# Optimization experiments

Measured on AMD Instinct MI355X. Metric: run time of the kernel, lower is better.

The kernel has to match this reference:

```python
import jax, jax.numpy as jnp
import numpy as np

D_MODEL = 1024
N_HEADS = 16
HEAD_DIM = D_MODEL // N_HEADS


def setup_inputs() -> dict:
    key = jax.random.key(0)
    ks = jax.random.split(key, 9)
    scale = 1.0 / np.sqrt(D_MODEL)
    x = jax.random.normal(ks[0], (2, 2048, D_MODEL), dtype=jnp.float32)
    Wq = jax.random.normal(ks[1], (D_MODEL, D_MODEL), dtype=jnp.float32) * scale
    bq = jax.random.normal(ks[2], (D_MODEL,), dtype=jnp.float32) * scale
    Wk = jax.random.normal(ks[3], (D_MODEL, D_MODEL), dtype=jnp.float32) * scale
    bk = jax.random.normal(ks[4], (D_MODEL,), dtype=jnp.float32) * scale
    Wv = jax.random.normal(ks[5], (D_MODEL, D_MODEL), dtype=jnp.float32) * scale
    bv = jax.random.normal(ks[6], (D_MODEL,), dtype=jnp.float32) * scale
    Wo = jax.random.normal(ks[7], (D_MODEL, D_MODEL), dtype=jnp.float32) * scale
    bo = jax.random.normal(ks[8], (D_MODEL,), dtype=jnp.float32) * scale
    return {"x": x, "Wq": Wq, "bq": bq, "Wk": Wk, "bk": bk,
            "Wv": Wv, "bv": bv, "Wo": Wo, "bo": bo}


def reference(x, Wq, bq, Wk, bk, Wv, bv, Wo, bo):
    B, S, _ = x.shape
    # projections: [B, S, D] -> [B, S, H, Dh]
    q = (x @ Wq + bq).reshape(B, S, N_HEADS, HEAD_DIM)
    k = (x @ Wk + bk).reshape(B, S, N_HEADS, HEAD_DIM)
    v = (x @ Wv + bv).reshape(B, S, N_HEADS, HEAD_DIM)
    inv_sqrt_d = jnp.float32(1.0 / np.sqrt(HEAD_DIM))
    # scores: [B, H, S, S]  (NOTE: source applies no causal mask despite name)
    scores = jnp.einsum('bqhd,bkhd->bhqk', q, k) * inv_sqrt_d
    attn = jax.nn.softmax(scores, axis=-1)
    out = jnp.einsum('bhqk,bkhd->bqhd', attn, v).reshape(B, S, D_MODEL)
    return out @ Wo + bo
```

## Files before the change

kernel.cpp:

```cpp
#include <hip/hip_runtime.h>

typedef __bf16 bf16x8 __attribute__((ext_vector_type(8)));
typedef float f32x4 __attribute__((ext_vector_type(4)));

#define D_MODEL 1024
#define SEQ 2048
#define NH 16
#define DH 64
#define MROWS 4096

__device__ __forceinline__ void load_lds16(const void* g, void* l) {
  __builtin_amdgcn_global_load_lds((__attribute__((address_space(1))) void*)g,
                                   (__attribute__((address_space(3))) void*)l, 16, 0, 0);
}

__device__ __forceinline__ f32x4 mfma16(bf16x8 a, bf16x8 b, f32x4 c) {
  return __builtin_amdgcn_mfma_f32_16x16x32_bf16(a, b, c, 0, 0, 0);
}

__device__ __forceinline__ unsigned pack2(float a, float b) {
  union { __bf16 h; unsigned short u; } pa, pb;
  pa.h = (__bf16)a; pb.h = (__bf16)b;
  return (unsigned)pa.u | ((unsigned)pb.u << 16);
}

__global__ __launch_bounds__(256) void cast_x_kernel(const float* __restrict__ X,
                                                     __bf16* __restrict__ Xb) {
  const size_t i = (size_t)blockIdx.x * 256 + threadIdx.x;
  const float4 a = reinterpret_cast<const float4*>(X)[i * 2];
  const float4 b = reinterpret_cast<const float4*>(X)[i * 2 + 1];
  bf16x8 o;
  o[0] = (__bf16)a.x; o[1] = (__bf16)a.y; o[2] = (__bf16)a.z; o[3] = (__bf16)a.w;
  o[4] = (__bf16)b.x; o[5] = (__bf16)b.y; o[6] = (__bf16)b.z; o[7] = (__bf16)b.w;
  *reinterpret_cast<bf16x8*>(Xb + i * 8) = o;
}

__global__ __launch_bounds__(256) void transpose_w(const float* __restrict__ W0, const float* __restrict__ W1,
                                                   const float* __restrict__ W2, const float* __restrict__ W3,
                                                   __bf16* __restrict__ WT) {
  __shared__ __bf16 tile[64][68];
  const int z = blockIdx.z;
  const float* W = z == 0 ? W0 : (z == 1 ? W1 : (z == 2 ? W2 : W3));
  const int r0 = blockIdx.x * 64;
  const int c0 = blockIdx.y * 64;
  const int tx = threadIdx.x & 63, ty = threadIdx.x >> 6;
#pragma unroll
  for (int i = 0; i < 16; ++i) {
    const int r = i * 4 + ty;
    tile[r][tx] = (__bf16)W[(size_t)(r0 + r) * D_MODEL + c0 + tx];
  }
  __syncthreads();
  __bf16* out = WT + (size_t)z * D_MODEL * D_MODEL;
#pragma unroll
  for (int i = 0; i < 16; ++i) {
    const int n = i * 4 + ty;
    out[(size_t)(c0 + n) * D_MODEL + r0 + tx] = tile[tx][n];
  }
}

template <int MODE>
__global__ __launch_bounds__(256) void gemm_bf16(
    const __bf16* __restrict__ A, const __bf16* __restrict__ BT,
    const float* __restrict__ bias0, const float* __restrict__ bias1, const float* __restrict__ bias2,
    __bf16* __restrict__ qout, __bf16* __restrict__ kout, __bf16* __restrict__ vout,
    float* __restrict__ fout) {
  __shared__ __bf16 As[128 * 32];
  __shared__ __bf16 Bs[128 * 32];
  const int t = threadIdx.x;
  const int l = t & 63;
  const int w = t >> 6;
  const int m0 = blockIdx.x * 128;
  const int n0 = blockIdx.y * 128;
  const int wr = w >> 1, wc = w & 1;
  const int l15 = l & 15, lhi = l >> 4;

  f32x4 acc[4][4] = {};

  const int srow = t >> 2;
  const int sslot = t & 3;

  for (int kt = 0; kt < D_MODEL / 32; ++kt) {
    const int kofs = kt * 32 + sslot * 8;
#pragma unroll
    for (int p = 0; p < 2; ++p) {
      load_lds16(A + (size_t)(m0 + p * 64 + srow) * D_MODEL + kofs, &As[(p * 64 + w * 16) * 32]);
      load_lds16(BT + (size_t)(n0 + p * 64 + srow) * D_MODEL + kofs, &Bs[(p * 64 + w * 16) * 32]);
    }
    __syncthreads();
    bf16x8 af[4], bfr[4];
#pragma unroll
    for (int i = 0; i < 4; ++i) {
      af[i] = *reinterpret_cast<const bf16x8*>(&As[(wr * 64 + i * 16 + l15) * 32 + lhi * 8]);
      bfr[i] = *reinterpret_cast<const bf16x8*>(&Bs[(wc * 64 + i * 16 + l15) * 32 + lhi * 8]);
    }
#pragma unroll
    for (int i = 0; i < 4; ++i)
#pragma unroll
      for (int j = 0; j < 4; ++j)
        acc[i][j] = mfma16(af[i], bfr[j], acc[i][j]);
    __syncthreads();
  }

  if (MODE == 0) {
#pragma unroll
    for (int j = 0; j < 4; ++j) {
      const int n = n0 + wc * 64 + j * 16 + l15;
      const int tsel = n >> 10;
      const int c = n & 1023;
      const float* bias = tsel == 0 ? bias0 : (tsel == 1 ? bias1 : bias2);
      const float bv = bias[c];
      const int h = c >> 6, dh = c & 63;
      if (tsel == 2) {
#pragma unroll
        for (int i = 0; i < 4; ++i) {
          const int mbase = m0 + wr * 64 + i * 16 + lhi * 4;
#pragma unroll
          for (int r = 0; r < 4; ++r) {
            const int mm = mbase + r;
            const int b = mm >> 11, s = mm & 2047;
            vout[((size_t)((b * NH + h) * DH + dh)) * SEQ + s] = (__bf16)(acc[i][j][r] + bv);
          }
        }
      } else {
        __bf16* dst = tsel == 0 ? qout : kout;
        const float scale = tsel == 0 ? 0.125f : 1.0f;
#pragma unroll
        for (int i = 0; i < 4; ++i) {
          const int mbase = m0 + wr * 64 + i * 16 + lhi * 4;
#pragma unroll
          for (int r = 0; r < 4; ++r) {
            const int mm = mbase + r;
            const int b = mm >> 11, s = mm & 2047;
            dst[((size_t)((b * NH + h) * SEQ + s)) * DH + dh] = (__bf16)((acc[i][j][r] + bv) * scale);
          }
        }
      }
    }
  } else {
#pragma unroll
    for (int j = 0; j < 4; ++j) {
      const int n = n0 + wc * 64 + j * 16 + l15;
      const float bv = bias0[n];
#pragma unroll
      for (int i = 0; i < 4; ++i) {
        const int mbase = m0 + wr * 64 + i * 16 + lhi * 4;
#pragma unroll
        for (int r = 0; r < 4; ++r)
          fout[(size_t)(mbase + r) * D_MODEL + n] = acc[i][j][r] + bv;
      }
    }
  }
}

__global__ __launch_bounds__(256) void flash_attn3(const __bf16* __restrict__ Q,
                                                   const __bf16* __restrict__ K,
                                                   const __bf16* __restrict__ VT,
                                                   __bf16* __restrict__ AO) {
  __shared__ __bf16 Kt[64 * 64];
  __shared__ __bf16 Vt[64 * 64];
  __shared__ __bf16 Pt[4][1024];
  const int t = threadIdx.x;
  const int l = t & 63, w = t >> 6;
  const int l15 = l & 15, lhi = l >> 4;

  const int fid = blockIdx.x;
  const int u = (fid & 7) * 128 + (fid >> 3);
  const int bh = u >> 5;
  const int qblk = u & 31;
  const int q0 = qblk * 64 + w * 16;

  const __bf16* Qb = Q + (size_t)bh * SEQ * DH;
  const __bf16* Kb = K + (size_t)bh * SEQ * DH;
  const __bf16* Vb = VT + (size_t)bh * DH * SEQ;

  bf16x8 qf[2];
#pragma unroll
  for (int kd = 0; kd < 2; ++kd)
    qf[kd] = *reinterpret_cast<const bf16x8*>(Qb + (size_t)(q0 + l15) * DH + kd * 32 + lhi * 8);

  f32x4 acc_o[4] = {};
  float mrun = -1e30f, lrun = 0.f;

  const int srow = l >> 3, sslot = l & 7;

  for (int kt = 0; kt < SEQ / 64; ++kt) {
    const int key0 = kt * 64;
#pragma unroll
    for (int pp = 0; pp < 2; ++pp) {
      const int p = w * 2 + pp;
      const int row = p * 8 + srow;
      const int sl = sslot ^ (row & 7);
      load_lds16(Kb + (size_t)(key0 + row) * DH + sl * 8, &Kt[p * 512]);
      load_lds16(Vb + (size_t)row * SEQ + key0 + sl * 8, &Vt[p * 512]);
    }
    __syncthreads();

    f32x4 s[4] = {};
#pragma unroll
    for (int kd = 0; kd < 2; ++kd)
#pragma unroll
      for (int kf = 0; kf < 4; ++kf) {
        const int key = kf * 16 + l15;
        const bf16x8 kfr = *reinterpret_cast<const bf16x8*>(
            &Kt[key * 64 + (((kd * 4 + lhi) ^ (key & 7)) << 3)]);
        s[kf] = mfma16(kfr, qf[kd], s[kf]);
      }

    float mt = s[0][0];
#pragma unroll
    for (int kf = 0; kf < 4; ++kf)
#pragma unroll
      for (int r = 0; r < 4; ++r) mt = fmaxf(mt, s[kf][r]);
    mt = fmaxf(mt, __shfl_xor(mt, 16));
    mt = fmaxf(mt, __shfl_xor(mt, 32));
    const float mnew = fmaxf(mrun, mt);
    const float alpha = __expf(mrun - mnew);
    float sum = 0.f;
#pragma unroll
    for (int kf = 0; kf < 4; ++kf)
#pragma unroll
      for (int r = 0; r < 4; ++r) {
        const float p = __expf(s[kf][r] - mnew);
        s[kf][r] = p;
        sum += p;
      }
    sum += __shfl_xor(sum, 16);
    sum += __shfl_xor(sum, 32);
    lrun = lrun * alpha + sum;
    mrun = mnew;
#pragma unroll
    for (int d0 = 0; d0 < 4; ++d0)
#pragma unroll
      for (int r = 0; r < 4; ++r) acc_o[d0][r] *= alpha;

#pragma unroll
    for (int kf = 0; kf < 4; ++kf) {
      uint2 wv;
      wv.x = pack2(s[kf][0], s[kf][1]);
      wv.y = pack2(s[kf][2], s[kf][3]);
      const int blk = (kf >> 1) * 4 + (kf & 1) * 2 + (lhi >> 1);
      const int dw = ((blk * 16 + l15) << 2) + ((lhi & 1) << 1);
      *reinterpret_cast<uint2*>(&Pt[w][dw * 2]) = wv;
    }

#pragma unroll
    for (int kc = 0; kc < 2; ++kc) {
      const bf16x8 pfr = *reinterpret_cast<const bf16x8*>(&Pt[w][((kc * 4 + lhi) * 16 + l15) * 8]);
#pragma unroll
      for (int d0 = 0; d0 < 4; ++d0) {
        const int dh = d0 * 16 + l15;
        const bf16x8 vfr = *reinterpret_cast<const bf16x8*>(
            &Vt[dh * 64 + (((kc * 4 + lhi) ^ (dh & 7)) << 3)]);
        acc_o[d0] = mfma16(vfr, pfr, acc_o[d0]);
      }
    }
    __syncthreads();
  }

  const int b = bh >> 4, h = bh & 15;
  const int s_ = q0 + l15;
  const float inv = 1.0f / lrun;
  __bf16* aorow = AO + ((size_t)(b * SEQ + s_)) * D_MODEL + h * DH;
#pragma unroll
  for (int d0 = 0; d0 < 4; ++d0) {
    const int dh0 = d0 * 16 + lhi * 4;
    uint2 pk;
    pk.x = pack2(acc_o[d0][0] * inv, acc_o[d0][1] * inv);
    pk.y = pack2(acc_o[d0][2] * inv, acc_o[d0][3] * inv);
    *reinterpret_cast<uint2*>(aorow + dh0) = pk;
  }
}

extern "C" void kernel_launch(void* const* d_in, const int* in_sizes, int n_in,
                              void* d_out, int out_size, void* d_ws, size_t ws_size,
                              hipStream_t stream) {
  (void)in_sizes; (void)n_in; (void)out_size; (void)ws_size;
  const float* x  = (const float*)d_in[0];
  const float* Wq = (const float*)d_in[1];
  const float* bq = (const float*)d_in[2];
  const float* Wk = (const float*)d_in[3];
  const float* bk = (const float*)d_in[4];
  const float* Wv = (const float*)d_in[5];
  const float* bv = (const float*)d_in[6];
  const float* Wo = (const float*)d_in[7];
  const float* bo = (const float*)d_in[8];
  float* out = (float*)d_out;
  char* ws = (char*)d_ws;
  __bf16* xb = (__bf16*)(ws);
  __bf16* WT = (__bf16*)(ws + (8u << 20));
  __bf16* qb = (__bf16*)(ws + (16u << 20));
  __bf16* kb = (__bf16*)(ws + (24u << 20));
  __bf16* vb = (__bf16*)(ws + (32u << 20));
  __bf16* ao = (__bf16*)(ws + (40u << 20));

  cast_x_kernel<<<dim3(2048), dim3(256), 0, stream>>>(x, xb);
  transpose_w<<<dim3(16, 16, 4), dim3(256), 0, stream>>>(Wq, Wk, Wv, Wo, WT);
  gemm_bf16<0><<<dim3(32, 24), dim3(256), 0, stream>>>(xb, WT, bq, bk, bv, qb, kb, vb, nullptr);
  flash_attn3<<<dim3(1024), dim3(256), 0, stream>>>(qb, kb, vb, ao);
  gemm_bf16<1><<<dim3(32, 8), dim3(256), 0, stream>>>(ao, WT + (size_t)3072 * 1024, bo,
                                                      nullptr, nullptr, nullptr, nullptr, nullptr, out);
}
```

Baseline: 229.6 us.

## Double-buffer attention K/V tiles, use exp2 with lazy rescaling, stage V-transpose store via LDS

Result: faster. 222.3 us (-3.2%).

```diff
diff --git a/kernel.cpp b/kernel.cpp
--- a/kernel.cpp
+++ b/kernel.cpp
@@ -8,6 +8,7 @@
 #define NH 16
 #define DH 64
 #define MROWS 4096
+#define LOG2E 1.44269504088896340736f
 
 __device__ __forceinline__ void load_lds16(const void* g, void* l) {
   __builtin_amdgcn_global_load_lds((__attribute__((address_space(1))) void*)g,
@@ -64,8 +65,9 @@
     const float* __restrict__ bias0, const float* __restrict__ bias1, const float* __restrict__ bias2,
     __bf16* __restrict__ qout, __bf16* __restrict__ kout, __bf16* __restrict__ vout,
     float* __restrict__ fout) {
-  __shared__ __bf16 As[128 * 32];
-  __shared__ __bf16 Bs[128 * 32];
+  __shared__ __bf16 sm[2][128 * 32];
+  __bf16* As = sm[0];
+  __bf16* Bs = sm[1];
   const int t = threadIdx.x;
   const int l = t & 63;
   const int w = t >> 6;
@@ -102,28 +104,52 @@
   }
 
   if (MODE == 0) {
-#pragma unroll
-    for (int j = 0; j < 4; ++j) {
-      const int n = n0 + wc * 64 + j * 16 + l15;
-      const int tsel = n >> 10;
-      const int c = n & 1023;
-      const float* bias = tsel == 0 ? bias0 : (tsel == 1 ? bias1 : bias2);
-      const float bv = bias[c];
-      const int h = c >> 6, dh = c & 63;
-      if (tsel == 2) {
-#pragma unroll
-        for (int i = 0; i < 4; ++i) {
-          const int mbase = m0 + wr * 64 + i * 16 + lhi * 4;
-#pragma unroll
-          for (int r = 0; r < 4; ++r) {
-            const int mm = mbase + r;
-            const int b = mm >> 11, s = mm & 2047;
-            vout[((size_t)((b * NH + h) * DH + dh)) * SEQ + s] = (__bf16)(acc[i][j][r] + bv);
+    if (n0 >= 2048) {
+      __bf16* Ts = sm[0];
+      char* Tsb = reinterpret_cast<char*>(Ts);
+      const int b = m0 >> 11, s0m = m0 & 2047;
+      const int c0p = n0 - 2048;
+#pragma unroll
+      for (int p = 0; p < 2; ++p) {
+        if (wc == p) {
+#pragma unroll
+          for (int j = 0; j < 4; ++j) {
+            const int cl = j * 16 + l15;
+            const float bv = bias2[c0p + p * 64 + cl];
+#pragma unroll
+            for (int i = 0; i < 4; ++i) {
+              const int sl = wr * 64 + i * 16 + lhi * 4;
+              uint2 wv;
+              wv.x = pack2(acc[i][j][0] + bv, acc[i][j][1] + bv);
+              wv.y = pack2(acc[i][j][2] + bv, acc[i][j][3] + bv);
+              const int bo = (cl * 256 + sl * 2) ^ ((cl & 7) << 4);
+              *reinterpret_cast<uint2*>(Tsb + bo) = wv;
+            }
           }
         }
-      } else {
+        __syncthreads();
+        const int c = t >> 2, ch = t & 3;
+        const int hh = (c0p + p * 64) >> 6;
+        __bf16* dst = vout + ((size_t)(b * NH + hh) * DH + c) * SEQ + s0m + ch * 32;
+#pragma unroll
+        for (int k2 = 0; k2 < 4; ++k2) {
+          const int bo = (c * 256 + ch * 64 + k2 * 16) ^ ((c & 7) << 4);
+          *reinterpret_cast<bf16x8*>(dst + k2 * 8) =
+              *reinterpret_cast<const bf16x8*>(Tsb + bo);
+        }
+        __syncthreads();
+      }
+    } else {
+#pragma unroll
+      for (int j = 0; j < 4; ++j) {
+        const int n = n0 + wc * 64 + j * 16 + l15;
+        const int tsel = n >> 10;
+        const int c = n & 1023;
+        const float* bias = tsel == 0 ? bias0 : bias1;
+        const float bv = bias[c];
         __bf16* dst = tsel == 0 ? qout : kout;
-        const float scale = tsel == 0 ? 0.125f : 1.0f;
+        const float scale = tsel == 0 ? (0.125f * LOG2E) : 1.0f;
+        const int h = c >> 6, dh = c & 63;
 #pragma unroll
         for (int i = 0; i < 4; ++i) {
           const int mbase = m0 + wr * 64 + i * 16 + lhi * 4;
@@ -152,12 +178,12 @@
   }
 }
 
-__global__ __launch_bounds__(256) void flash_attn3(const __bf16* __restrict__ Q,
+__global__ __launch_bounds__(256) void flash_attn4(const __bf16* __restrict__ Q,
                                                    const __bf16* __restrict__ K,
                                                    const __bf16* __restrict__ VT,
                                                    __bf16* __restrict__ AO) {
-  __shared__ __bf16 Kt[64 * 64];
-  __shared__ __bf16 Vt[64 * 64];
+  __shared__ __bf16 Kt[2][64 * 64];
+  __shared__ __bf16 Vt[2][64 * 64];
   __shared__ __bf16 Pt[4][1024];
   const int t = threadIdx.x;
   const int l = t & 63, w = t >> 6;
@@ -179,87 +205,122 @@
     qf[kd] = *reinterpret_cast<const bf16x8*>(Qb + (size_t)(q0 + l15) * DH + kd * 32 + lhi * 8);
 
   f32x4 acc_o[4] = {};
-  float mrun = -1e30f, lrun = 0.f;
+  float mrun = -1e30f, lpart = 0.f;
 
   const int srow = l >> 3, sslot = l & 7;
 
+  int koffb[8];
+#pragma unroll
+  for (int kd = 0; kd < 2; ++kd)
+#pragma unroll
+    for (int kf = 0; kf < 4; ++kf) {
+      const int key = kf * 16 + l15;
+      koffb[kd * 4 + kf] = (key * 64 + (((kd * 4 + lhi) ^ (key & 7)) << 3)) * 2;
+    }
+  int voffb[8];
+#pragma unroll
+  for (int kc = 0; kc < 2; ++kc)
+#pragma unroll
+    for (int d0 = 0; d0 < 4; ++d0) {
+      const int dh = d0 * 16 + l15;
+      voffb[kc * 4 + d0] = (dh * 64 + (((kc * 4 + lhi) ^ (dh & 7)) << 3)) * 2;
+    }
+  int pwoff[4];
+#pragma unroll
+  for (int kf = 0; kf < 4; ++kf) {
+    const int blk = (kf >> 1) * 4 + (kf & 1) * 2 + (lhi >> 1);
+    pwoff[kf] = (((blk * 16 + l15) << 2) + ((lhi & 1) << 1)) * 4;
+  }
+  int proff[2];
+#pragma unroll
+  for (int kc = 0; kc < 2; ++kc) proff[kc] = ((kc * 4 + lhi) * 16 + l15) * 16;
+  char* Ptb = reinterpret_cast<char*>(&Pt[w][0]);
+
+  const int row0 = (w * 2 + 0) * 8 + srow, row1 = (w * 2 + 1) * 8 + srow;
+  const __bf16* kp0 = Kb + (size_t)row0 * DH + (sslot ^ (row0 & 7)) * 8;
+  const __bf16* kp1 = Kb + (size_t)row1 * DH + (sslot ^ (row1 & 7)) * 8;
+  const __bf16* vp0 = Vb + (size_t)row0 * SEQ + (sslot ^ (row0 & 7)) * 8;
+  const __bf16* vp1 = Vb + (size_t)row1 * SEQ + (sslot ^ (row1 & 7)) * 8;
+  const int ldsA = (w * 2 + 0) * 512, ldsB = (w * 2 + 1) * 512;
+
+  load_lds16(kp0, &Kt[0][ldsA]); kp0 += 64 * DH;
+  load_lds16(kp1, &Kt[0][ldsB]); kp1 += 64 * DH;
+  load_lds16(vp0, &Vt[0][ldsA]); vp0 += 64;
+  load_lds16(vp1, &Vt[0][ldsB]); vp1 += 64;
+
   for (int kt = 0; kt < SEQ / 64; ++kt) {
-    const int key0 = kt * 64;
-#pragma unroll
-    for (int pp = 0; pp < 2; ++pp) {
-      const int p = w * 2 + pp;
-      const int row = p * 8 + srow;
-      const int sl = sslot ^ (row & 7);
-      load_lds16(Kb + (size_t)(key0 + row) * DH + sl * 8, &Kt[p * 512]);
-      load_lds16(Vb + (size_t)row * SEQ + key0 + sl * 8, &Vt[p * 512]);
-    }
+    const int cur = kt & 1;
     __syncthreads();
+    if (kt + 1 < SEQ / 64) {
+      const int nb = cur ^ 1;
+      load_lds16(kp0, &Kt[nb][ldsA]); kp0 += 64 * DH;
+      load_lds16(kp1, &Kt[nb][ldsB]); kp1 += 64 * DH;
+      load_lds16(vp0, &Vt[nb][ldsA]); vp0 += 64;
+      load_lds16(vp1, &Vt[nb][ldsB]); vp1 += 64;
+    }
+    const char* Kc = reinterpret_cast<const char*>(&Kt[cur][0]);
+    const char* Vc = reinterpret_cast<const char*>(&Vt[cur][0]);
 
     f32x4 s[4] = {};
 #pragma unroll
     for (int kd = 0; kd < 2; ++kd)
 #pragma unroll
       for (int kf = 0; kf < 4; ++kf) {
-        const int key = kf * 16 + l15;
-        const bf16x8 kfr = *reinterpret_cast<const bf16x8*>(
-            &Kt[key * 64 + (((kd * 4 + lhi) ^ (key & 7)) << 3)]);
+        const bf16x8 kfr = *reinterpret_cast<const bf16x8*>(Kc + koffb[kd * 4 + kf]);
         s[kf] = mfma16(kfr, qf[kd], s[kf]);
       }
 
-    float mt = s[0][0];
-#pragma unroll
-    for (int kf = 0; kf < 4; ++kf)
-#pragma unroll
-      for (int r = 0; r < 4; ++r) mt = fmaxf(mt, s[kf][r]);
+    float mt = fmaxf(fmaxf(s[0][0], s[0][1]), fmaxf(s[0][2], s[0][3]));
+#pragma unroll
+    for (int kf = 1; kf < 4; ++kf)
+      mt = fmaxf(mt, fmaxf(fmaxf(s[kf][0], s[kf][1]), fmaxf(s[kf][2], s[kf][3])));
     mt = fmaxf(mt, __shfl_xor(mt, 16));
     mt = fmaxf(mt, __shfl_xor(mt, 32));
-    const float mnew = fmaxf(mrun, mt);
-    const float alpha = __expf(mrun - mnew);
+    if (mt > mrun + 8.f) {
+      const float alpha = __builtin_amdgcn_exp2f(mrun - mt);
+      lpart *= alpha;
+#pragma unroll
+      for (int d0 = 0; d0 < 4; ++d0)
+#pragma unroll
+        for (int r = 0; r < 4; ++r) acc_o[d0][r] *= alpha;
+      mrun = mt;
+    }
     float sum = 0.f;
 #pragma unroll
     for (int kf = 0; kf < 4; ++kf)
 #pragma unroll
       for (int r = 0; r < 4; ++r) {
-        const float p = __expf(s[kf][r] - mnew);
+        const float p = __builtin_amdgcn_exp2f(s[kf][r] - mrun);
         s[kf][r] = p;
         sum += p;
       }
-    sum += __shfl_xor(sum, 16);
-    sum += __shfl_xor(sum, 32);
-    lrun = lrun * alpha + sum;
-    mrun = mnew;
-#pragma unroll
-    for (int d0 = 0; d0 < 4; ++d0)
-#pragma unroll
-      for (int r = 0; r < 4; ++r) acc_o[d0][r] *= alpha;
+    lpart += sum;
 
 #pragma unroll
     for (int kf = 0; kf < 4; ++kf) {
       uint2 wv;
       wv.x = pack2(s[kf][0], s[kf][1]);
       wv.y = pack2(s[kf][2], s[kf][3]);
-      const int blk = (kf >> 1) * 4 + (kf & 1) * 2 + (lhi >> 1);
-      const int dw = ((blk * 16 + l15) << 2) + ((lhi & 1) << 1);
-      *reinterpret_cast<uint2*>(&Pt[w][dw * 2]) = wv;
+      *reinterpret_cast<uint2*>(Ptb + pwoff[kf]) = wv;
     }
 
 #pragma unroll
     for (int kc = 0; kc < 2; ++kc) {
-      const bf16x8 pfr = *reinterpret_cast<const bf16x8*>(&Pt[w][((kc * 4 + lhi) * 16 + l15) * 8]);
+      const bf16x8 pfr = *reinterpret_cast<const bf16x8*>(Ptb + proff[kc]);
 #pragma unroll
       for (int d0 = 0; d0 < 4; ++d0) {
-        const int dh = d0 * 16 + l15;
-        const bf16x8 vfr = *reinterpret_cast<const bf16x8*>(
-            &Vt[dh * 64 + (((kc * 4 + lhi) ^ (dh & 7)) << 3)]);
+        const bf16x8 vfr = *reinterpret_cast<const bf16x8*>(Vc + voffb[kc * 4 + d0]);
         acc_o[d0] = mfma16(vfr, pfr, acc_o[d0]);
       }
     }
-    __syncthreads();
-  }
-
+  }
+
+  float lsum = lpart;
+  lsum += __shfl_xor(lsum, 16);
+  lsum += __shfl_xor(lsum, 32);
+  const float inv = 1.0f / lsum;
   const int b = bh >> 4, h = bh & 15;
   const int s_ = q0 + l15;
-  const float inv = 1.0f / lrun;
   __bf16* aorow = AO + ((size_t)(b * SEQ + s_)) * D_MODEL + h * DH;
 #pragma unroll
   for (int d0 = 0; d0 < 4; ++d0) {
@@ -296,7 +357,7 @@
   cast_x_kernel<<<dim3(2048), dim3(256), 0, stream>>>(x, xb);
   transpose_w<<<dim3(16, 16, 4), dim3(256), 0, stream>>>(Wq, Wk, Wv, Wo, WT);
   gemm_bf16<0><<<dim3(32, 24), dim3(256), 0, stream>>>(xb, WT, bq, bk, bv, qb, kb, vb, nullptr);
-  flash_attn3<<<dim3(1024), dim3(256), 0, stream>>>(qb, kb, vb, ao);
+  flash_attn4<<<dim3(1024), dim3(256), 0, stream>>>(qb, kb, vb, ao);
   gemm_bf16<1><<<dim3(32, 8), dim3(256), 0, stream>>>(ao, WT + (size_t)3072 * 1024, bo,
                                                       nullptr, nullptr, nullptr, nullptr, nullptr, out);
 }
```
